# Optimization experiments

Hardware: AMD Instinct MI355X
Metric: run time of the kernel (lower is better)

The kernel has to match this reference:

```python
import jax, jax.numpy as jnp
import numpy as np

NF = 64
DG = 8
NB = 5
K = 3
K2 = K * K


def conv2d(x, w, b):
    # x: [B,C,H,W], w: [O,I,3,3] -> SAME padding, stride 1
    y = jax.lax.conv_general_dilated(x, w, (1, 1), 'SAME',
                                     dimension_numbers=('NCHW', 'OIHW', 'NCHW'))
    return y + b[None, :, None, None]


def dcn(x, off_feat, cw, cb, w, b):
    """Modulated deformable conv (DCNv2, extra_offset_mask=True).
    x: [B,C,H,W] sampled input; off_feat: [B,C,H,W] feeds conv_offset_mask.
    cw/cb: offset-mask conv params [3*DG*K2, C, 3, 3]; w/b: main conv [O, C, 3, 3].
    """
    B, C, H, W = x.shape
    Cg = C // DG
    om = conv2d(off_feat, cw, cb)                      # [B, 3*DG*K2, H, W]
    o1, o2, m = jnp.split(om, 3, axis=1)
    dy = o1.reshape(B, DG, K2, H, W)
    dx = o2.reshape(B, DG, K2, H, W)
    mask = jax.nn.sigmoid(m).reshape(B, DG, K2, H, W)
    # kernel tap offsets for 3x3, pad=1, dilation=1
    kyy, kxx = np.meshgrid(np.arange(K) - 1, np.arange(K) - 1, indexing='ij')
    ky = jnp.asarray(kyy.reshape(K2), x.dtype)
    kx = jnp.asarray(kxx.reshape(K2), x.dtype)
    gy = jnp.arange(H, dtype=x.dtype)
    gx = jnp.arange(W, dtype=x.dtype)
    py = gy[None, None, None, :, None] + ky[None, None, :, None, None] + dy  # [B,DG,K2,H,W]
    px = gx[None, None, None, None, :] + kx[None, None, :, None, None] + dx
    y0 = jnp.floor(py)
    x0 = jnp.floor(px)
    wy = py - y0
    wx = px - x0
    y0i = y0.astype(jnp.int32)
    x0i = x0.astype(jnp.int32)
    xg = x.reshape(B, DG, Cg, H * W)

    def gather(iy, ix):
        valid = ((iy >= 0) & (iy < H) & (ix >= 0) & (ix < W)).astype(x.dtype)
        lin = (jnp.clip(iy, 0, H - 1) * W + jnp.clip(ix, 0, W - 1)).reshape(B, DG, 1, K2 * H * W)
        v = jnp.take_along_axis(xg, jnp.broadcast_to(lin, (B, DG, Cg, K2 * H * W)), axis=3)
        return v.reshape(B, DG, Cg, K2, H, W) * valid[:, :, None]

    v00 = gather(y0i, x0i)
    v01 = gather(y0i, x0i + 1)
    v10 = gather(y0i + 1, x0i)
    v11 = gather(y0i + 1, x0i + 1)
    wy_ = wy[:, :, None]
    wx_ = wx[:, :, None]
    val = (v00 * (1 - wy_) * (1 - wx_) + v01 * (1 - wy_) * wx_
           + v10 * wy_ * (1 - wx_) + v11 * wy_ * wx_) * mask[:, :, None]  # [B,DG,Cg,K2,H,W]
    wr = w.reshape(w.shape[0], DG, Cg, K2)
    out = jnp.einsum('bgckhw,ogck->bohw', val, wr) + b[None, :, None, None]
    return out


def setup_inputs() -> dict:
    key = jax.random.key(0)
    ks = jax.random.split(key, 16)

    def w_(k, shape, s=0.05):
        return jax.random.normal(k, shape, jnp.float32) * s

    B, N, C, H, W = 4, 5, 1, 128, 128
    inp = {}
    inp['x'] = jax.random.normal(ks[0], (B, N, C, H, W), jnp.float32)
    inp['w_init'] = w_(ks[1], (NF, C, 3, 3))
    inp['b_init'] = jnp.zeros((NF,), jnp.float32)
    inp['res_w1'] = w_(ks[2], (NB, NF, NF, 3, 3))
    inp['res_b1'] = jnp.zeros((NB, NF), jnp.float32)
    inp['res_w2'] = w_(ks[3], (NB, NF, NF, 3, 3))
    inp['res_b2'] = jnp.zeros((NB, NF), jnp.float32)
    inp['w_bn'] = w_(ks[4], (NF, 2 * NF, 3, 3))
    inp['b_bn'] = jnp.zeros((NF,), jnp.float32)
    inp['off_w'] = w_(ks[5], (4, NF, NF, 3, 3))
    inp['off_b'] = jnp.zeros((4, NF), jnp.float32)
    inp['com_w'] = w_(ks[6], (4, 3 * DG * K2, NF, 3, 3), 0.01)
    inp['com_b'] = jnp.zeros((4, 3 * DG * K2), jnp.float32)
    inp['dcn_w'] = w_(ks[7], (4, NF, NF, 3, 3))
    inp['dcn_b'] = jnp.zeros((4, NF), jnp.float32)
    inp['w_rec'] = w_(ks[8], (C, NF, 3, 3))
    inp['b_rec'] = jnp.zeros((C,), jnp.float32)
    return inp


def reference(x, w_init, b_init, res_w1, res_b1, res_w2, res_b2, w_bn, b_bn,
              off_w, off_b, com_w, com_b, dcn_w, dcn_b, w_rec, b_rec):
    B, N, C, H, W = x.shape
    y = x.reshape(B * N, C, H, W)
    out = jax.nn.relu(conv2d(y, w_init, b_init))
    for i in range(NB):  # ResidualBlock_noBN x nb
        h = jax.nn.relu(conv2d(out, res_w1[i], res_b1[i]))
        out = out + conv2d(h, res_w2[i], res_b2[i])
    out = out.reshape(B, N, NF, H, W)
    ref = out[:, N // 2]
    ys = []
    for i in range(N):
        nei = out[:, i]
        fea = conv2d(jnp.concatenate([ref, nei], axis=1), w_bn, b_bn)
        o = conv2d(fea, off_w[0], off_b[0])
        fea = dcn(fea, o, com_w[0], com_b[0], dcn_w[0], dcn_b[0])
        o = conv2d(fea, off_w[1], off_b[1])
        fea = dcn(fea, o, com_w[1], com_b[1], dcn_w[1], dcn_b[1])
        o = conv2d(fea, off_w[2], off_b[2])
        fea = dcn(nei, o, com_w[2], com_b[2], dcn_w[2], dcn_b[2])
        o = conv2d(fea, off_w[3], off_b[3])
        aligned = dcn(fea, o, com_w[3], com_b[3], dcn_w[3], dcn_b[3])
        ys.append(conv2d(aligned, w_rec, b_rec))
    return jnp.concatenate(ys, axis=1)  # [B, N*C, H, W]
```

## Files before the change

### kernel.cpp

```cpp
#include <hip/hip_runtime.h>
#include <hip/hip_bf16.h>

typedef __hip_bfloat16 bf16;
typedef __attribute__((ext_vector_type(8))) short short8;
typedef __attribute__((ext_vector_type(4))) float floatx4;
typedef unsigned short ush;

#define HH 128
#define WW 128
#define HW 16384

__device__ __forceinline__ float b2f(bf16 v){ return __bfloat162float(v); }
__device__ __forceinline__ float bfu2f(ush u){
  union{unsigned int i; float f;} c; c.i = ((unsigned int)u)<<16; return c.f;
}
__device__ __forceinline__ ush f2bfu(float f){
  bf16 h = __float2bfloat16(f);
  return *(ush*)&h;
}

__global__ void detect_dtype(const ush* __restrict__ x, float* __restrict__ flag){
  __shared__ int bad;
  if (threadIdx.x==0) bad = 0;
  __syncthreads();
  for (int j=threadIdx.x; j<4096; j+=256){
    float f = bfu2f(x[j]);
    if (!(fabsf(f) < 1e4f)) atomicOr(&bad, 1);
  }
  __syncthreads();
  if (threadIdx.x==0) flag[0] = bad ? 0.f : 1.f;
}

__global__ void convert_in(const void* __restrict__ src, float* __restrict__ dst, int n,
                           const float* __restrict__ flag){
  int i = blockIdx.x*256 + threadIdx.x;
  if (i >= n) return;
  float v = (flag[0] > 0.5f) ? b2f(((const bf16*)src)[i]) : ((const float*)src)[i];
  dst[i] = v;
}

__global__ void transpose_w(const float* __restrict__ src, float* __restrict__ dst, int Co, int CiK){
  int tid = blockIdx.x*256 + threadIdx.x;
  if (tid >= Co*CiK) return;
  int co = tid / CiK, r = tid - co*CiK;
  dst[(long)r*Co + co] = src[tid];
}

__global__ void pack_w2(const float* __restrict__ src, ush* __restrict__ dst,
                        int Cout, int Cin, int kh, int nOcB){
  int idx = blockIdx.x*256 + threadIdx.x;
  int total = nOcB*36864;
  if (idx >= total) return;
  int ocb = idx / 36864; int r = idx - ocb*36864;
  int c  = r & 7;
  int lx = (r>>3) & 15;
  int n  = (r>>7) & 3;
  int lk = (r>>9) & 3;
  int j  = r>>11;
  int t = j>>1, ch = j&1;
  int oc = n*16+lx;
  int k = ch*32 + lk*8 + c;
  int ocg = ocb*64 + oc, icg = kh*64 + k;
  float v = (ocg < Cout && icg < Cin) ? src[((long)ocg*Cin + icg)*9 + t] : 0.f;
  dst[idx] = f2bfu(v);
}

__global__ void pack_dcn_w(const float* __restrict__ src, ush* __restrict__ dst){
  int idx = blockIdx.x*256 + threadIdx.x;
  if (idx >= 49152) return;
  int g = idx / 6144; int r = idx - g*6144;
  int oc = r / 96; int k = r - oc*96;
  float v = 0.f;
  if (k < 72){
    int tap = k >> 3, c = k & 7;
    v = src[((long)oc*64 + g*8 + c)*9 + tap];
  }
  dst[idx] = f2bfu(v);
}

__global__ __launch_bounds__(256) void conv_init_kernel(const float* __restrict__ x,
    const float* __restrict__ wT, const float* __restrict__ bias,
    ush* __restrict__ fh, ush* __restrict__ fl){
  __shared__ ush L[256*66];
  int tid = threadIdx.x;
  int tx = tid & 15, ty = tid >> 4;
  int gx = blockIdx.x*16+tx, gy = blockIdx.y*16+ty;
  int n = blockIdx.z;
  const float* xp = x + (long)n*HW;
  float v[9];
  #pragma unroll
  for (int dy=0;dy<3;dy++)
    #pragma unroll
    for (int dx=0;dx<3;dx++){
      int yy = gy+dy-1, xx = gx+dx-1;
      bool ok = (yy>=0)&&(yy<HH)&&(xx>=0)&&(xx<WW);
      v[dy*3+dx] = ok ? xp[yy*WW+xx] : 0.f;
    }
  float acc[64];
  #pragma unroll 1
  for (int oc=0; oc<64; oc++){
    float a = bias[oc];
    #pragma unroll
    for (int k=0;k<9;k++) a = fmaf(v[k], wT[k*64+oc], a);
    acc[oc] = fmaxf(a, 0.f);
  }
  #pragma unroll 1
  for (int pass=0; pass<2; pass++){
    #pragma unroll 1
    for (int oc=0; oc<64; oc++){
      float a = acc[oc];
      ush h = f2bfu(a);
      L[tid*66+oc] = pass ? f2bfu(a - bfu2f(h)) : h;
    }
    __syncthreads();
    ush* dst = pass ? fl : fh;
    for (int j=tid; j<2048; j+=256){
      int c8 = j&7, pidx = j>>3;
      int row = pidx>>4, col = pidx&15;
      long addr = ((long)n*HW + (blockIdx.y*16+row)*WW + blockIdx.x*16+col)*64 + c8*8;
      *(short8*)(dst+addr) = *(const short8*)(L + pidx*66 + c8*8);
    }
    __syncthreads();
  }
}

template<int NPL, int MINW, int MT>
__global__ __launch_bounds__(256, MINW) void conv_mfma(
    const ush* __restrict__ in_hi, const ush* __restrict__ in_lo, long in_ps,
    const ush* __restrict__ in2_hi, const ush* __restrict__ in2_lo, long in2_ps,
    const ush* __restrict__ wpack, const ush* __restrict__ wpack2,
    const float* __restrict__ bias, int has_bias,
    const ush* __restrict__ add_hi, const ush* __restrict__ add_lo,
    long add_ps, int add_cs,
    ush* __restrict__ out_hi, ush* __restrict__ out_lo,
    long out_ps, int out_cs,
    float* __restrict__ out_pf, int pf_C,
    int Cout, int nOcB, int relu)
{
  constexpr int ROWS = 4*MT + 2;
  constexpr int APX  = ROWS*18;
  constexpr int NPX  = 4*MT*16;
  constexpr int LDSN = (NPL*APX*64 > 2*NPX*66) ? NPL*APX*64 : 2*NPX*66;
  __shared__ ush A[LDSN];
  int tid = threadIdx.x;
  int z = blockIdx.z; int img = z / nOcB; int ocb = z - img*nOcB;
  int x0 = blockIdx.x*16 - 1, y0 = blockIdx.y*(4*MT) - 1;
  int w = tid>>6, l = tid&63, lx = l&15, lk = l>>4;
  floatx4 acc[MT][4];
  #pragma unroll
  for (int mt=0;mt<MT;mt++)
    #pragma unroll
    for (int n=0;n<4;n++) acc[mt][n] = (floatx4){0.f,0.f,0.f,0.f};

  auto phase = [&](const ush* ihb, const ush* ilb, const ush* wfb){
    __syncthreads();
    #pragma unroll
    for (int p=0;p<NPL;p++){
      const ush* src = p ? ilb : ihb;
      ush* dstp = A + p*APX*64;
      for (int j=tid; j<APX*8; j+=256){
        int pidx = j>>3, c8 = j&7;
        int row = pidx/18, col = pidx - row*18;
        int yy = y0+row, xx = x0+col;
        uint4 v = make_uint4(0u,0u,0u,0u);
        if ((unsigned)yy < 128u && (unsigned)xx < 128u)
          v = *(const uint4*)(src + ((long)(yy*WW+xx))*64 + c8*8);
        *(uint4*)(dstp + pidx*64 + ((c8 ^ (pidx&7))<<3)) = v;
      }
    }
    const ush* wfrag = wfb + lk*4*128 + lx*8;
    short8 bf[4][4];
    #pragma unroll
    for (int s=0;s<3;s++)
      #pragma unroll
      for (int n=0;n<4;n++)
        bf[s][n] = *(const short8*)(wfrag + (s*16 + n)*128);
    __syncthreads();
    #pragma unroll
    for (int j=0;j<18;j++){
      int t = j>>1, ch = j&1;
      if (j<15){
        #pragma unroll
        for (int n=0;n<4;n++)
          bf[(j+3)&3][n] = *(const short8*)(wfrag + ((j+3)*16 + n)*128);
      }
      int ky = t/3, kx = t - ky*3;
      int jc = ch*4 + lk;
      #pragma unroll
      for (int mt=0; mt<MT; mt++){
        int pidx = (w*MT+mt+ky)*18 + lx + kx;
        #pragma unroll
        for (int p=0;p<NPL;p++){
          short8 af = *(const short8*)(A + p*APX*64 + pidx*64 + ((jc ^ (pidx&7))<<3));
          #pragma unroll
          for (int n=0;n<4;n++)
            acc[mt][n] = __builtin_amdgcn_mfma_f32_16x16x32_bf16(af, bf[j&3][n], acc[mt][n], 0,0,0);
        }
      }
    }
  };
  phase(in_hi + (long)img*in_ps*64, in_lo + (long)img*in_ps*64,
        wpack + (long)ocb*36864);
  if (wpack2)
    phase(in2_hi + (long)img*in2_ps*64, in2_lo + (long)img*in2_ps*64,
          wpack2 + (long)ocb*36864);

  int ybase = blockIdx.y*(4*MT) + w*MT;
  int xbase = blockIdx.x*16 + lk*4;
  if (out_pf){
    #pragma unroll
    for (int mt=0;mt<MT;mt++){
      int y = ybase + mt;
      #pragma unroll
      for (int n=0;n<4;n++){
        int ocg = ocb*64 + n*16 + lx;
        if (ocg < Cout){
          float bv = has_bias ? bias[ocg] : 0.f;
          #pragma unroll
          for (int r=0;r<4;r++){
            int xg = xbase + r;
            out_pf[((long)img*pf_C + ocg)*HW + y*WW + xg] = acc[mt][n][r] + bv;
          }
        }
      }
    }
  } else {
    __syncthreads();
    ush* L0 = A;
    ush* L1 = A + NPX*66;
    #pragma unroll
    for (int mt=0;mt<MT;mt++){
      int y = ybase + mt;
      int rowl = w*MT + mt;
      #pragma unroll
      for (int n=0;n<4;n++){
        int ocg = n*16 + lx;
        float bv = has_bias ? bias[ocg] : 0.f;
        #pragma unroll
        for (int r=0;r<4;r++){
          int coll = lk*4 + r;
          float v = acc[mt][n][r] + bv;
          if (add_hi){
            long ap = ((long)img*add_ps + y*WW + blockIdx.x*16 + coll)*add_cs + ocg;
            v += bfu2f(add_hi[ap]) + bfu2f(add_lo[ap]);
          }
          if (relu) v = fmaxf(v, 0.f);
          ush h = f2bfu(v);
          L0[(rowl*16+coll)*66 + ocg] = h;
          if (out_lo) L1[(rowl*16+coll)*66 + ocg] = f2bfu(v - bfu2f(h));
        }
      }
    }
    __syncthreads();
    for (int j=tid; j<NPX*8; j+=256){
      int pidx = j>>3, c8 = j&7;
      int row = pidx>>4, col = pidx&15;
      long pp = (long)img*out_ps + (blockIdx.y*(4*MT)+row)*WW + blockIdx.x*16+col;
      *(short8*)(out_hi + pp*64 + c8*8) = *(const short8*)(L0 + pidx*66 + c8*8);
      if (out_lo)
        *(short8*)(out_lo + pp*64 + c8*8) = *(const short8*)(L1 + pidx*66 + c8*8);
    }
  }
}

__global__ __launch_bounds__(256) void repack_gp(const ush* __restrict__ in_h,
    const ush* __restrict__ in_l, long in_ps, float* __restrict__ gp){
  long idx = (long)blockIdx.x*256 + threadIdx.x;
  int img = (int)(idx >> 17);
  int rem = (int)(idx & 131071);
  int pix = rem >> 3, c8 = rem & 7;
  long src = ((long)img*in_ps + pix)*64 + c8*8;
  short8 h = *(const short8*)(in_h+src);
  short8 lo = *(const short8*)(in_l+src);
  float* d = gp + (((long)(img*8+c8))*HW + pix)*8;
  #pragma unroll
  for (int c=0;c<8;c++) d[c] = bfu2f((ush)h[c]) + bfu2f((ush)lo[c]);
}

__global__ __launch_bounds__(256) void dcn_mfma(
    const float* __restrict__ gp,
    const float* __restrict__ om,
    const ush* __restrict__ wpk,
    const float* __restrict__ bias,
    ush* __restrict__ out_hi, ush* __restrict__ out_lo)
{
  __shared__ ush S[19968];
  ush* Ah = S;
  ush* Bt = S + 13312;
  int tid = threadIdx.x;
  int gy = blockIdx.x, img = blockIdx.y;
  {
    short8 z = {0,0,0,0,0,0,0,0};
    for (int j=tid; j<384; j+=256){
      int px = j/3, c = j - px*3;
      *(short8*)(Ah + px*104 + 72 + c*8) = z;
    }
  }
  int w = tid>>6, l = tid&63, lx = l&15, lk = l>>4;
  int px_s = tid & 127, hf = tid >> 7;
  const float* omb = om + (long)img*216*HW + gy*WW + px_s;
  floatx4 acc[2][4];
  #pragma unroll
  for (int mt=0;mt<2;mt++)
    #pragma unroll
    for (int n=0;n<4;n++) acc[mt][n] = (floatx4){0.f,0.f,0.f,0.f};

  #pragma unroll 1
  for (int g=0; g<8; g++){
    __syncthreads();
    const ush* wsrc = wpk + g*6144;
    for (int j=tid; j<768; j+=256){
      int oc = j/12, kc = j - oc*12;
      *(short8*)(Bt + oc*104 + kc*8) = *(const short8*)(wsrc + oc*96 + kc*8);
    }
    const float* gpb = gp + ((long)(img*8+g))*HW*8;
    int t0 = hf ? 5 : 0, t1 = hf ? 9 : 5;
    #pragma unroll 1
    for (int t=t0; t<t1; t++){
      int ch = g*9+t;
      float dy = omb[(long)ch*HW];
      float dx = omb[(long)(72+ch)*HW];
      float mv = omb[(long)(144+ch)*HW];
      float m = 1.f/(1.f+__expf(-mv));
      float py = (float)gy + (float)(t/3 - 1) + dy;
      float pxf = (float)px_s + (float)(t%3 - 1) + dx;
      float fy = floorf(py), fx = floorf(pxf);
      int y0 = (int)fy, x0 = (int)fx;
      float wy = py - fy, wx = pxf - fx;
      bool y0v = (y0>=0 && y0<HH), y1v = (y0+1>=0 && y0+1<HH);
      bool x0v = (x0>=0 && x0<WW), x1v = (x0+1>=0 && x0+1<WW);
      float w00 = (1.f-wy)*(1.f-wx)*m * ((y0v&&x0v)?1.f:0.f);
      float w01 = (1.f-wy)*wx*m      * ((y0v&&x1v)?1.f:0.f);
      float w10 = wy*(1.f-wx)*m      * ((y1v&&x0v)?1.f:0.f);
      float w11 = wy*wx*m            * ((y1v&&x1v)?1.f:0.f);
      int y0c = min(max(y0,0),HH-1), y1c = min(max(y0+1,0),HH-1);
      int x0c = min(max(x0,0),WW-1), x1c = min(max(x0+1,0),WW-1);
      const float* p00 = gpb + (((long)(y0c*WW+x0c))<<3);
      const float* p01 = gpb + (((long)(y0c*WW+x1c))<<3);
      const float* p10 = gpb + (((long)(y1c*WW+x0c))<<3);
      const float* p11 = gpb + (((long)(y1c*WW+x1c))<<3);
      float4 a00=*(const float4*)p00, b00=*(const float4*)(p00+4);
      float4 a01=*(const float4*)p01, b01=*(const float4*)(p01+4);
      float4 a10=*(const float4*)p10, b10=*(const float4*)(p10+4);
      float4 a11=*(const float4*)p11, b11=*(const float4*)(p11+4);
      float val[8];
      val[0]=w00*a00.x+w01*a01.x+w10*a10.x+w11*a11.x;
      val[1]=w00*a00.y+w01*a01.y+w10*a10.y+w11*a11.y;
      val[2]=w00*a00.z+w01*a01.z+w10*a10.z+w11*a11.z;
      val[3]=w00*a00.w+w01*a01.w+w10*a10.w+w11*a11.w;
      val[4]=w00*b00.x+w01*b01.x+w10*b10.x+w11*b11.x;
      val[5]=w00*b00.y+w01*b01.y+w10*b10.y+w11*b11.y;
      val[6]=w00*b00.z+w01*b01.z+w10*b10.z+w11*b11.z;
      val[7]=w00*b00.w+w01*b01.w+w10*b10.w+w11*b11.w;
      short8 vh;
      #pragma unroll
      for (int c=0;c<8;c++) vh[c] = (short)f2bfu(val[c]);
      *(short8*)(Ah + px_s*104 + t*8) = vh;
    }
    __syncthreads();
    #pragma unroll
    for (int ks=0; ks<3; ks++){
      short8 bfg[4];
      #pragma unroll
      for (int n=0;n<4;n++)
        bfg[n] = *(const short8*)(Bt + (n*16+lx)*104 + ks*32 + lk*8);
      #pragma unroll
      for (int mt=0; mt<2; mt++){
        int px = (w*2+mt)*16 + lx;
        short8 ah = *(const short8*)(Ah + px*104 + ks*32 + lk*8);
        #pragma unroll
        for (int n=0;n<4;n++)
          acc[mt][n] = __builtin_amdgcn_mfma_f32_16x16x32_bf16(ah, bfg[n], acc[mt][n], 0,0,0);
      }
    }
  }
  __syncthreads();
  ush* L0 = S;
  ush* L1 = S + 128*66;
  #pragma unroll
  for (int mt=0;mt<2;mt++){
    #pragma unroll
    for (int n=0;n<4;n++){
      int oc = n*16 + lx;
      float bv = bias[oc];
      #pragma unroll
      for (int r=0;r<4;r++){
        int pxl = (w*2+mt)*16 + lk*4 + r;
        float v = acc[mt][n][r] + bv;
        ush h = f2bfu(v);
        L0[pxl*66 + oc] = h;
        L1[pxl*66 + oc] = f2bfu(v - bfu2f(h));
      }
    }
  }
  __syncthreads();
  long base = ((long)img*HW + gy*WW)*64;
  for (int j=tid; j<1024; j+=256){
    int pidx = j>>3, c8 = j&7;
    *(short8*)(out_hi + base + pidx*64 + c8*8) = *(const short8*)(L0 + pidx*66 + c8*8);
    *(short8*)(out_lo + base + pidx*64 + c8*8) = *(const short8*)(L1 + pidx*66 + c8*8);
  }
}

__global__ __launch_bounds__(256) void rec_kernel(
    const ush* __restrict__ fh, const ush* __restrict__ fl,
    const float* __restrict__ wT, const float* __restrict__ bias,
    void* __restrict__ out, int ni, const float* __restrict__ flag){
  __shared__ float red[256];
  int tid = threadIdx.x;
  int p = tid & 31, q = tid >> 5;
  int gx = blockIdx.x*32 + p;
  int gy = blockIdx.y;
  int b = blockIdx.z;
  float acc = 0.f;
  #pragma unroll
  for (int t=0;t<9;t++){
    int yy = gy + t/3 - 1, xx = gx + t%3 - 1;
    if (yy<0||yy>=HH||xx<0||xx>=WW) continue;
    long base = ((long)b*HW + yy*WW + xx)*64 + q*8;
    short8 h = *(const short8*)(fh + base);
    short8 lo = *(const short8*)(fl + base);
    #pragma unroll
    for (int cc=0;cc<8;cc++){
      float v = bfu2f((ush)h[cc]) + bfu2f((ush)lo[cc]);
      acc = fmaf(v, wT[(q*8+cc)*9 + t], acc);
    }
  }
  red[q*32+p] = acc;
  __syncthreads();
  if (tid < 32){
    float s = bias[0];
    #pragma unroll
    for (int k=0;k<8;k++) s += red[k*32+tid];
    long idx = ((long)b*5+ni)*HW + gy*WW + blockIdx.x*32 + tid;
    if (flag[0] > 0.5f) ((bf16*)out)[idx] = __float2bfloat16(s);
    else                ((float*)out)[idx] = s;
  }
}

extern "C" void kernel_launch(void* const* d_in, const int* in_sizes, int n_in,
                              void* d_out, int out_size, void* d_ws, size_t ws_size,
                              hipStream_t stream) {
  float* ws = (float*)d_ws;

  size_t off = 16;
  auto alloc = [&](size_t nel){ size_t o = off; off += (nel + 7) & ~(size_t)7; return o; };

  static const int IN_N[17] = {327680, 576, 64, 184320, 320, 184320, 320,
                               73728, 64, 147456, 256, 497664, 864, 147456,
                               256, 576, 1};
  size_t cin[17];
  for (int i=0;i<17;i++) cin[i] = alloc(IN_N[i]);

  size_t wt_init = alloc(640);
  size_t wdcn_pk[4]; for (int s=0;s<4;s++) wdcn_pk[s] = alloc(24576);
  size_t wt_rec = alloc(640);
  size_t pk_res1[5], pk_res2[5];
  for (int i=0;i<5;i++) pk_res1[i] = alloc(18432);
  for (int i=0;i<5;i++) pk_res2[i] = alloc(18432);
  size_t pk_bn[2]; for (int h=0;h<2;h++) pk_bn[h] = alloc(18432);
  size_t pk_off[4]; for (int s=0;s<4;s++) pk_off[s] = alloc(18432);
  size_t pk_com[4]; for (int s=0;s<4;s++) pk_com[s] = alloc(73728);

  size_t feat_h_o = alloc(10485760);
  size_t feat_l_o = alloc(10485760);
  size_t U = alloc(26738688);

  ush* feat_h = (ush*)(ws + feat_h_o);
  ush* feat_l = (ush*)(ws + feat_l_o);
  ush* feaA_h = (ush*)(ws + U);
  ush* feaA_l = (ush*)(ws + U + 2097152);
  ush* feaB_h = (ush*)(ws + U + 4194304);
  ush* feaB_l = (ush*)(ws + U + 6291456);
  ush* obuf_h = (ush*)(ws + U + 8388608);
  float* gpbuf = ws + U + 8388608;
  float* ombuf = ws + U + 12582912;
  ush* hbuf_h = (ush*)(ws + U);

  float* flag = ws;

  detect_dtype<<<dim3(1), dim3(256), 0, stream>>>((const ush*)d_in[0], flag);
  for (int i=0;i<17;i++){
    int n = IN_N[i];
    convert_in<<<dim3((n+255)/256), dim3(256), 0, stream>>>(d_in[i], ws+cin[i], n, flag);
  }
  const float* b_init = ws+cin[2];
  const float* res_b1 = ws+cin[4];
  const float* res_b2 = ws+cin[6];
  const float* b_bn   = ws+cin[8];
  const float* off_b  = ws+cin[10];
  const float* com_b  = ws+cin[12];
  const float* dcn_b  = ws+cin[14];
  const float* b_rec  = ws+cin[16];

  auto tr = [&](size_t src_o, size_t dst_o, int Co, int CiK){
    int total = Co*CiK;
    transpose_w<<<dim3((total+255)/256), dim3(256), 0, stream>>>(ws+src_o, ws+dst_o, Co, CiK);
  };
  tr(cin[1], wt_init, 64, 9);
  tr(cin[15], wt_rec, 1, 576);
  for (int s=0;s<4;s++)
    pack_dcn_w<<<dim3(192), dim3(256), 0, stream>>>(ws+cin[13]+(size_t)s*36864,
                                                    (ush*)(ws+wdcn_pk[s]));

  auto pack = [&](size_t src_o, size_t dst_o, int Cout, int Cin, int kh, int nOcB){
    int total = nOcB*36864;
    pack_w2<<<dim3((total+255)/256), dim3(256), 0, stream>>>(
        ws+src_o, (ush*)(ws+dst_o), Cout, Cin, kh, nOcB);
  };
  for (int i=0;i<5;i++) pack(cin[3]+(size_t)i*36864, pk_res1[i], 64, 64, 0, 1);
  for (int i=0;i<5;i++) pack(cin[5]+(size_t)i*36864, pk_res2[i], 64, 64, 0, 1);
  for (int h=0;h<2;h++) pack(cin[7], pk_bn[h], 64, 128, h, 1);
  for (int s=0;s<4;s++) pack(cin[9]+(size_t)s*36864,  pk_off[s], 64, 64, 0, 1);
  for (int s=0;s<4;s++) pack(cin[11]+(size_t)s*124416, pk_com[s], 216, 64, 0, 4);

  dim3 cblk(256);
  auto conv = [&](const ush* in_h, const ush* in_l, long in_ps,
                  const ush* in2_h, const ush* in2_l, long in2_ps,
                  size_t pk, const ush* pk2p,
                  const float* bias, int has_bias,
                  const ush* add_h, const ush* add_l, long add_ps, int add_cs,
                  ush* o_h, ush* o_l, long out_ps, int out_cs,
                  float* o_pf, int pf_C,
                  int Cout, int nOcB, int relu, int N, int nPl, int mtMode){
    if (nPl == 2 && mtMode == 2)
      conv_mfma<2,2,2><<<dim3(8,16,N*nOcB), cblk, 0, stream>>>(
          in_h, in_l, in_ps, in2_h, in2_l, in2_ps,
          (const ush*)(ws+pk), pk2p, bias, has_bias,
          add_h, add_l, add_ps, add_cs, o_h, o_l, out_ps, out_cs,
          o_pf, pf_C, Cout, nOcB, relu);
    else if (nPl == 2 && mtMode == 1)
      conv_mfma<2,2,1><<<dim3(8,32,N*nOcB), cblk, 0, stream>>>(
          in_h, in_l, in_ps, in2_h, in2_l, in2_ps,
          (const ush*)(ws+pk), pk2p, bias, has_bias,
          add_h, add_l, add_ps, add_cs, o_h, o_l, out_ps, out_cs,
          o_pf, pf_C, Cout, nOcB, relu);
    else
      conv_mfma<1,3,2><<<dim3(8,16,N*nOcB), cblk, 0, stream>>>(
          in_h, in_l, in_ps, in2_h, in2_l, in2_ps,
          (const ush*)(ws+pk), pk2p, bias, has_bias,
          add_h, add_l, add_ps, add_cs, o_h, o_l, out_ps, out_cs,
          o_pf, pf_C, Cout, nOcB, relu);
  };

  conv_init_kernel<<<dim3(8,8,20), cblk, 0, stream>>>(ws+cin[0], ws+wt_init, b_init,
                                                      feat_h, feat_l);
  for (int i=0;i<5;i++){
    conv(feat_h, feat_l, HW, nullptr, nullptr, 0, pk_res1[i], nullptr,
         res_b1+(size_t)i*64, 1,
         nullptr, nullptr, 0, 0, hbuf_h, nullptr, HW, 64, nullptr, 0, 64, 1, 1, 20, 2, 2);
    conv(hbuf_h, hbuf_h, HW, nullptr, nullptr, 0, pk_res2[i], nullptr,
         res_b2+(size_t)i*64, 1,
         feat_h, feat_l, HW, 64, feat_h, feat_l, HW, 64, nullptr, 0, 64, 1, 0, 20, 1, 2);
  }
  for (int i=0;i<5;i++){
    conv(feat_h + (size_t)2*HW*64, feat_l + (size_t)2*HW*64, 5L*HW,
         feat_h + (size_t)i*HW*64, feat_l + (size_t)i*HW*64, 5L*HW,
         pk_bn[0], (const ush*)(ws+pk_bn[1]), b_bn, 1,
         nullptr, nullptr, 0, 0, feaA_h, feaA_l, HW, 64, nullptr, 0, 64, 1, 0, 4, 2, 1);
    ush *fa_h = feaA_h, *fa_l = feaA_l, *fb_h = feaB_h, *fb_l = feaB_l;
    for (int s=0;s<4;s++){
      conv(fa_h, fa_l, HW, nullptr, nullptr, 0, pk_off[s], nullptr,
           off_b+(size_t)s*64, 1,
           nullptr, nullptr, 0, 0, obuf_h, nullptr, HW, 64, nullptr, 0, 64, 1, 0, 4, 2, 1);
      conv(obuf_h, obuf_h, HW, nullptr, nullptr, 0, pk_com[s], nullptr,
           com_b+(size_t)s*216, 1,
           nullptr, nullptr, 0, 0, nullptr, nullptr, 0, 0, ombuf, 216, 216, 4, 0, 4, 1, 2);
      const ush *xs_h, *xs_l; long xps;
      if (s == 2){ xs_h = feat_h + (size_t)i*HW*64; xs_l = feat_l + (size_t)i*HW*64; xps = 5L*HW; }
      else       { xs_h = fa_h;                     xs_l = fa_l;                     xps = HW; }
      repack_gp<<<dim3(2048), cblk, 0, stream>>>(xs_h, xs_l, xps, gpbuf);
      dcn_mfma<<<dim3(128,4), cblk, 0, stream>>>(gpbuf, ombuf,
          (const ush*)(ws+wdcn_pk[s]), dcn_b+(size_t)s*64, fb_h, fb_l);
      ush* t;
      t = fa_h; fa_h = fb_h; fb_h = t;
      t = fa_l; fa_l = fb_l; fb_l = t;
    }
    rec_kernel<<<dim3(4,128,4), cblk, 0, stream>>>(fa_h, fa_l, ws+wt_rec, b_rec, d_out, i, flag);
  }
}
```

Measured before the change: 3.598 ms.

## Split DCN blocks into half-rows and use single-plane/smaller-tile conv variants

After: 3.436 ms. 1.05x faster.

```diff
diff --git a/kernel.cpp b/kernel.cpp
--- a/kernel.cpp
+++ b/kernel.cpp
@@ -284,26 +284,26 @@
     const float* __restrict__ bias,
     ush* __restrict__ out_hi, ush* __restrict__ out_lo)
 {
-  __shared__ ush S[19968];
+  __shared__ ush S[13312];
   ush* Ah = S;
-  ush* Bt = S + 13312;
+  ush* Bt = S + 6656;
   int tid = threadIdx.x;
-  int gy = blockIdx.x, img = blockIdx.y;
+  int half = blockIdx.x, gy = blockIdx.y, img = blockIdx.z;
+  int xoff = half*64;
   {
     short8 z = {0,0,0,0,0,0,0,0};
-    for (int j=tid; j<384; j+=256){
+    for (int j=tid; j<192; j+=256){
       int px = j/3, c = j - px*3;
       *(short8*)(Ah + px*104 + 72 + c*8) = z;
     }
   }
   int w = tid>>6, l = tid&63, lx = l&15, lk = l>>4;
-  int px_s = tid & 127, hf = tid >> 7;
-  const float* omb = om + (long)img*216*HW + gy*WW + px_s;
-  floatx4 acc[2][4];
+  int px_s = tid & 63, q = tid >> 6;
+  int t0 = (q==0)?0:(q*2+1), t1 = t0 + ((q==0)?3:2);
+  const float* omb = om + (long)img*216*HW + gy*WW + xoff + px_s;
+  floatx4 acc[4];
   #pragma unroll
-  for (int mt=0;mt<2;mt++)
-    #pragma unroll
-    for (int n=0;n<4;n++) acc[mt][n] = (floatx4){0.f,0.f,0.f,0.f};
+  for (int n=0;n<4;n++) acc[n] = (floatx4){0.f,0.f,0.f,0.f};
 
   #pragma unroll 1
   for (int g=0; g<8; g++){
@@ -314,7 +314,6 @@
       *(short8*)(Bt + oc*104 + kc*8) = *(const short8*)(wsrc + oc*96 + kc*8);
     }
     const float* gpb = gp + ((long)(img*8+g))*HW*8;
-    int t0 = hf ? 5 : 0, t1 = hf ? 9 : 5;
     #pragma unroll 1
     for (int t=t0; t<t1; t++){
       int ch = g*9+t;
@@ -323,7 +322,7 @@
       float mv = omb[(long)(144+ch)*HW];
       float m = 1.f/(1.f+__expf(-mv));
       float py = (float)gy + (float)(t/3 - 1) + dy;
-      float pxf = (float)px_s + (float)(t%3 - 1) + dx;
+      float pxf = (float)(xoff + px_s) + (float)(t%3 - 1) + dx;
       float fy = floorf(py), fx = floorf(pxf);
       int y0 = (int)fy, x0 = (int)fx;
       float wy = py - fy, wx = pxf - fx;
@@ -364,38 +363,32 @@
       #pragma unroll
       for (int n=0;n<4;n++)
         bfg[n] = *(const short8*)(Bt + (n*16+lx)*104 + ks*32 + lk*8);
-      #pragma unroll
-      for (int mt=0; mt<2; mt++){
-        int px = (w*2+mt)*16 + lx;
-        short8 ah = *(const short8*)(Ah + px*104 + ks*32 + lk*8);
-        #pragma unroll
-        for (int n=0;n<4;n++)
-          acc[mt][n] = __builtin_amdgcn_mfma_f32_16x16x32_bf16(ah, bfg[n], acc[mt][n], 0,0,0);
-      }
+      int px = w*16 + lx;
+      short8 ah = *(const short8*)(Ah + px*104 + ks*32 + lk*8);
+      #pragma unroll
+      for (int n=0;n<4;n++)
+        acc[n] = __builtin_amdgcn_mfma_f32_16x16x32_bf16(ah, bfg[n], acc[n], 0,0,0);
     }
   }
   __syncthreads();
   ush* L0 = S;
-  ush* L1 = S + 128*66;
+  ush* L1 = S + 64*66;
   #pragma unroll
-  for (int mt=0;mt<2;mt++){
-    #pragma unroll
-    for (int n=0;n<4;n++){
-      int oc = n*16 + lx;
-      float bv = bias[oc];
-      #pragma unroll
-      for (int r=0;r<4;r++){
-        int pxl = (w*2+mt)*16 + lk*4 + r;
-        float v = acc[mt][n][r] + bv;
-        ush h = f2bfu(v);
-        L0[pxl*66 + oc] = h;
-        L1[pxl*66 + oc] = f2bfu(v - bfu2f(h));
-      }
+  for (int n=0;n<4;n++){
+    int oc = n*16 + lx;
+    float bv = bias[oc];
+    #pragma unroll
+    for (int r=0;r<4;r++){
+      int pxl = w*16 + lk*4 + r;
+      float v = acc[n][r] + bv;
+      ush h = f2bfu(v);
+      L0[pxl*66 + oc] = h;
+      L1[pxl*66 + oc] = f2bfu(v - bfu2f(h));
     }
   }
   __syncthreads();
-  long base = ((long)img*HW + gy*WW)*64;
-  for (int j=tid; j<1024; j+=256){
+  long base = ((long)img*HW + gy*WW + xoff)*64;
+  for (int j=tid; j<512; j+=256){
     int pidx = j>>3, c8 = j&7;
     *(short8*)(out_hi + base + pidx*64 + c8*8) = *(const short8*)(L0 + pidx*66 + c8*8);
     *(short8*)(out_lo + base + pidx*64 + c8*8) = *(const short8*)(L1 + pidx*66 + c8*8);
@@ -535,6 +528,12 @@
           (const ush*)(ws+pk), pk2p, bias, has_bias,
           add_h, add_l, add_ps, add_cs, o_h, o_l, out_ps, out_cs,
           o_pf, pf_C, Cout, nOcB, relu);
+    else if (nPl == 1 && mtMode == 1)
+      conv_mfma<1,3,1><<<dim3(8,32,N*nOcB), cblk, 0, stream>>>(
+          in_h, in_l, in_ps, in2_h, in2_l, in2_ps,
+          (const ush*)(ws+pk), pk2p, bias, has_bias,
+          add_h, add_l, add_ps, add_cs, o_h, o_l, out_ps, out_cs,
+          o_pf, pf_C, Cout, nOcB, relu);
     else
       conv_mfma<1,3,2><<<dim3(8,16,N*nOcB), cblk, 0, stream>>>(
           in_h, in_l, in_ps, in2_h, in2_l, in2_ps,
@@ -548,10 +547,10 @@
   for (int i=0;i<5;i++){
     conv(feat_h, feat_l, HW, nullptr, nullptr, 0, pk_res1[i], nullptr,
          res_b1+(size_t)i*64, 1,
-         nullptr, nullptr, 0, 0, hbuf_h, nullptr, HW, 64, nullptr, 0, 64, 1, 1, 20, 2, 2);
+         nullptr, nullptr, 0, 0, hbuf_h, nullptr, HW, 64, nullptr, 0, 64, 1, 1, 20, 2, 1);
     conv(hbuf_h, hbuf_h, HW, nullptr, nullptr, 0, pk_res2[i], nullptr,
          res_b2+(size_t)i*64, 1,
-         feat_h, feat_l, HW, 64, feat_h, feat_l, HW, 64, nullptr, 0, 64, 1, 0, 20, 1, 2);
+         feat_h, feat_l, HW, 64, feat_h, feat_l, HW, 64, nullptr, 0, 64, 1, 0, 20, 1, 1);
   }
   for (int i=0;i<5;i++){
     conv(feat_h + (size_t)2*HW*64, feat_l + (size_t)2*HW*64, 5L*HW,
@@ -560,9 +559,9 @@
          nullptr, nullptr, 0, 0, feaA_h, feaA_l, HW, 64, nullptr, 0, 64, 1, 0, 4, 2, 1);
     ush *fa_h = feaA_h, *fa_l = feaA_l, *fb_h = feaB_h, *fb_l = feaB_l;
     for (int s=0;s<4;s++){
-      conv(fa_h, fa_l, HW, nullptr, nullptr, 0, pk_off[s], nullptr,
+      conv(fa_h, fa_h, HW, nullptr, nullptr, 0, pk_off[s], nullptr,
            off_b+(size_t)s*64, 1,
-           nullptr, nullptr, 0, 0, obuf_h, nullptr, HW, 64, nullptr, 0, 64, 1, 0, 4, 2, 1);
+           nullptr, nullptr, 0, 0, obuf_h, nullptr, HW, 64, nullptr, 0, 64, 1, 0, 4, 1, 1);
       conv(obuf_h, obuf_h, HW, nullptr, nullptr, 0, pk_com[s], nullptr,
            com_b+(size_t)s*216, 1,
            nullptr, nullptr, 0, 0, nullptr, nullptr, 0, 0, ombuf, 216, 216, 4, 0, 4, 1, 2);
@@ -570,7 +569,7 @@
       if (s == 2){ xs_h = feat_h + (size_t)i*HW*64; xs_l = feat_l + (size_t)i*HW*64; xps = 5L*HW; }
       else       { xs_h = fa_h;                     xs_l = fa_l;                     xps = HW; }
       repack_gp<<<dim3(2048), cblk, 0, stream>>>(xs_h, xs_l, xps, gpbuf);
-      dcn_mfma<<<dim3(128,4), cblk, 0, stream>>>(gpbuf, ombuf,
+      dcn_mfma<<<dim3(2,128,4), cblk, 0, stream>>>(gpbuf, ombuf,
           (const ush*)(ws+wdcn_pk[s]), dcn_b+(size_t)s*64, fb_h, fb_l);
       ush* t;
       t = fa_h; fa_h = fb_h; fb_h = t;
```
